# Performance work log

Hardware: AMD Instinct MI355X
Metric: run time of the kernel (lower is better)

## Reference

```python
import jax, jax.numpy as jnp
import numpy as np

# Sampled-neighborhood sizes (NeighborSampler-style shrinking hops)
N0, N1, N2, N3 = 200000, 50000, 12500, 3200
E0, E1, E2 = 500000, 125000, 32000
D_IN, D_H, D_OUT = 128, 256, 128


def setup_inputs() -> dict:
    key = jax.random.key(0)
    ks = jax.random.split(key, 16)
    x = jax.random.normal(ks[0], (N0, D_IN), dtype=jnp.float32)
    src0 = jax.random.randint(ks[1], (E0,), 0, N0)
    dst0 = jax.random.randint(ks[2], (E0,), 0, N1)
    src1 = jax.random.randint(ks[3], (E1,), 0, N1)
    dst1 = jax.random.randint(ks[4], (E1,), 0, N2)
    src2 = jax.random.randint(ks[5], (E2,), 0, N2)
    dst2 = jax.random.randint(ks[6], (E2,), 0, N3)
    s = 0.05
    # SAGEConv params: lin_l (applied to aggregated neighbors, has bias), lin_r (root)
    wl0 = jax.random.normal(ks[7], (D_H, D_IN), dtype=jnp.float32) * s
    wr0 = jax.random.normal(ks[8], (D_H, D_IN), dtype=jnp.float32) * s
    b0 = jnp.zeros((D_H,), dtype=jnp.float32)
    wl1 = jax.random.normal(ks[9], (D_H, D_H), dtype=jnp.float32) * s
    wr1 = jax.random.normal(ks[10], (D_H, D_H), dtype=jnp.float32) * s
    b1 = jnp.zeros((D_H,), dtype=jnp.float32)
    wl2 = jax.random.normal(ks[11], (D_OUT, D_H), dtype=jnp.float32) * s
    wr2 = jax.random.normal(ks[12], (D_OUT, D_H), dtype=jnp.float32) * s
    b2 = jnp.zeros((D_OUT,), dtype=jnp.float32)
    return {"x": x, "src0": src0, "dst0": dst0, "src1": src1, "dst1": dst1,
            "src2": src2, "dst2": dst2,
            "wl0": wl0, "wr0": wr0, "b0": b0,
            "wl1": wl1, "wr1": wr1, "b1": b1,
            "wl2": wl2, "wr2": wr2, "b2": b2}


def _sage(x, src, dst, n_tgt, wl, wr, b):
    """Bipartite SAGEConv with mean aggregation (PyG default)."""
    x_tgt = x[:n_tgt]                                   # [n_tgt, d_in]
    msg = x[src]                                        # [E, d_in] gather
    s = jax.ops.segment_sum(msg, dst, num_segments=n_tgt)
    cnt = jax.ops.segment_sum(jnp.ones((src.shape[0], 1), x.dtype), dst,
                              num_segments=n_tgt)
    mean = s / jnp.maximum(cnt, 1.0)                    # mean over in-neighbors
    return mean @ wl.T + b + x_tgt @ wr.T               # [n_tgt, d_out]


def reference(x, src0, dst0, src1, dst1, src2, dst2,
              wl0, wr0, b0, wl1, wr1, b1, wl2, wr2, b2):
    h = jax.nn.relu(_sage(x, src0, dst0, N1, wl0, wr0, b0))
    h = jax.nn.relu(_sage(h, src1, dst1, N2, wl1, wr1, b1))
    return _sage(h, src2, dst2, N3, wl2, wr2, b2)       # [N3, D_OUT]
```

## Files before the change

kernel.cpp:

```cpp
#include <hip/hip_runtime.h>

#define N0s 200000
#define N1s 50000
#define N2s 12500
#define N3s 3200
#define E0s 500000
#define E1s 125000
#define E2s 32000
#define D_INs 128
#define D_Hs 256
#define D_OUTs 128

#define CAP 32
#define LOGCAP 5

#define GSTRIDE 72

#define WN4 65536
#define WCAST_BLOCKS 32
#define FILLE_BLOCKS ((E0s + E1s + E2s + 255) / 256)

typedef __attribute__((ext_vector_type(8))) short short8;
typedef __attribute__((ext_vector_type(8))) unsigned short ushort8;
typedef __attribute__((ext_vector_type(4))) float floatx4;

__device__ __forceinline__ unsigned short f32_to_bf16_rne(float f) {
    unsigned int u = __float_as_uint(f);
    u += 0x7fffu + ((u >> 16) & 1u);
    return (unsigned short)(u >> 16);
}
__device__ __forceinline__ float bf16_to_f32(unsigned short h) {
    return __uint_as_float(((unsigned int)h) << 16);
}

struct PrepArgs {
    const int *src0, *dst0, *src1, *dst1, *src2, *dst2;
    int *cnt0, *cnt1, *cnt2;
    int *eidx0, *eidx1, *eidx2;
    const float* ws_[6]; unsigned short* wd[6];
};

__launch_bounds__(256)
__global__ void fill3w(PrepArgs a)
{
    if (blockIdx.x < FILLE_BLOCKS) {
        int e = blockIdx.x * 256 + threadIdx.x;
        if (e < E0s) {
            int d = a.dst0[e];
            int p = atomicAdd(&a.cnt0[d], 1);
            if (p < CAP) a.eidx0[(d << LOGCAP) + p] = a.src0[e];
        } else if (e < E0s + E1s) {
            int i = e - E0s;
            int d = a.dst1[i];
            int p = atomicAdd(&a.cnt1[d], 1);
            if (p < CAP) a.eidx1[(d << LOGCAP) + p] = a.src1[i];
        } else if (e < E0s + E1s + E2s) {
            int i = e - E0s - E1s;
            int d = a.dst2[i];
            int p = atomicAdd(&a.cnt2[d], 1);
            if (p < CAP) a.eidx2[(d << LOGCAP) + p] = a.src2[i];
        }
        return;
    }
    int cb = blockIdx.x - FILLE_BLOCKS;
    #pragma unroll
    for (int j = 0; j < 8; ++j) {
        int g = cb * 2048 + j * 256 + threadIdx.x;
        if (g < WN4) {
            int seg, base;
            if      (g < 8192)  { seg = 0; base = 0; }
            else if (g < 16384) { seg = 1; base = 8192; }
            else if (g < 32768) { seg = 2; base = 16384; }
            else if (g < 49152) { seg = 3; base = 32768; }
            else if (g < 57344) { seg = 4; base = 49152; }
            else                { seg = 5; base = 57344; }
            int k = g - base;
            float4 v = *(const float4*)&a.ws_[seg][(size_t)k * 4];
            ushort4 o;
            o.x = f32_to_bf16_rne(v.x);
            o.y = f32_to_bf16_rne(v.y);
            o.z = f32_to_bf16_rne(v.z);
            o.w = f32_to_bf16_rne(v.w);
            *(ushort4*)&a.wd[seg][(size_t)k * 4] = o;
        }
    }
}

__launch_bounds__(256)
__global__ void gather_mean_f32(const float* __restrict__ X,
                                const int* __restrict__ eidx,
                                const int* __restrict__ cnt,
                                unsigned short* __restrict__ out,
                                int n_tgt)
{
    int gid = blockIdx.x * 256 + threadIdx.x;
    int row = gid >> 5;
    if (row >= n_tgt) return;
    int c = (gid & 31) << 2;

    int deg = cnt[row];
    int e = min(deg, CAP);
    const int* bp = &eidx[row << LOGCAP];

    float a0 = 0.f, a1 = 0.f, a2 = 0.f, a3 = 0.f;
    int i = 0;
    for (; i + 4 <= e; i += 4) {
        int4 ss = *(const int4*)&bp[i];
        float4 v0 = *(const float4*)&X[(size_t)ss.x * D_INs + c];
        float4 v1 = *(const float4*)&X[(size_t)ss.y * D_INs + c];
        float4 v2 = *(const float4*)&X[(size_t)ss.z * D_INs + c];
        float4 v3 = *(const float4*)&X[(size_t)ss.w * D_INs + c];
        a0 += (v0.x + v1.x) + (v2.x + v3.x);
        a1 += (v0.y + v1.y) + (v2.y + v3.y);
        a2 += (v0.z + v1.z) + (v2.z + v3.z);
        a3 += (v0.w + v1.w) + (v2.w + v3.w);
    }
    for (; i < e; ++i) {
        float4 v = *(const float4*)&X[(size_t)bp[i] * D_INs + c];
        a0 += v.x; a1 += v.y; a2 += v.z; a3 += v.w;
    }
    float inv = 1.0f / fmaxf((float)deg, 1.0f);
    ushort4 o;
    o.x = f32_to_bf16_rne(a0 * inv);
    o.y = f32_to_bf16_rne(a1 * inv);
    o.z = f32_to_bf16_rne(a2 * inv);
    o.w = f32_to_bf16_rne(a3 * inv);
    *(ushort4*)&out[(size_t)row * D_INs + c] = o;
}

__launch_bounds__(256)
__global__ void gather_mean(const unsigned short* __restrict__ X,
                            const int* __restrict__ eidx,
                            const int* __restrict__ cnt,
                            unsigned short* __restrict__ out,
                            int n_tgt, int D, int shift)
{
    int gid = blockIdx.x * 256 + threadIdx.x;
    int row = gid >> shift;
    if (row >= n_tgt) return;
    int c = (gid & ((1 << shift) - 1)) << 3;

    int deg = cnt[row];
    int e = min(deg, CAP);
    const int* bp = &eidx[row << LOGCAP];

    float acc[8];
    #pragma unroll
    for (int j = 0; j < 8; ++j) acc[j] = 0.f;

    int i = 0;
    for (; i + 4 <= e; i += 4) {
        int4 ss = *(const int4*)&bp[i];
        ushort8 v0 = *(const ushort8*)&X[(size_t)ss.x * D + c];
        ushort8 v1 = *(const ushort8*)&X[(size_t)ss.y * D + c];
        ushort8 v2 = *(const ushort8*)&X[(size_t)ss.z * D + c];
        ushort8 v3 = *(const ushort8*)&X[(size_t)ss.w * D + c];
        #pragma unroll
        for (int j = 0; j < 8; ++j)
            acc[j] += (bf16_to_f32(v0[j]) + bf16_to_f32(v1[j]))
                    + (bf16_to_f32(v2[j]) + bf16_to_f32(v3[j]));
    }
    for (; i < e; ++i) {
        ushort8 v0 = *(const ushort8*)&X[(size_t)bp[i] * D + c];
        #pragma unroll
        for (int j = 0; j < 8; ++j) acc[j] += bf16_to_f32(v0[j]);
    }

    float inv = 1.0f / fmaxf((float)deg, 1.0f);
    ushort8 o;
    #pragma unroll
    for (int j = 0; j < 8; ++j) o[j] = f32_to_bf16_rne(acc[j] * inv);
    *(ushort8*)&out[(size_t)row * D + c] = o;
}

template<int BM, int BN, int OUT_BF16, int RELU, int A2F32>
__launch_bounds__(256)
__global__ void mfma_gemm_t(const unsigned short* __restrict__ A1,
                            const unsigned short* __restrict__ A2,
                            const float* __restrict__ A2f,
                            const unsigned short* __restrict__ W1,
                            const unsigned short* __restrict__ W2,
                            const float* __restrict__ bias,
                            void* __restrict__ Cout,
                            int M, int N, int K1, int K2)
{
    constexpr int MT = BM / 32;
    constexpr int NT = BN / 32;
    constexpr int AITER_A = BM / 32;
    constexpr int AITER_B = BN / 32;
    constexpr int CS = BN + 4;
    constexpr int STAGE_SH = (BM + BN) * GSTRIDE;
    constexpr int CS_SH = OUT_BF16 ? BM * CS : 0;
    constexpr int SMEM_SH = STAGE_SH > CS_SH ? STAGE_SH : CS_SH;

    __shared__ unsigned short smem[SMEM_SH];
    unsigned short* As = smem;
    unsigned short* Bs = smem + BM * GSTRIDE;

    const int tid  = threadIdx.x;
    const int wave = tid >> 6;
    const int lane = tid & 63;
    const int quad = lane >> 4;
    const int lr   = lane & 15;
    const int wm   = wave >> 1;
    const int wn   = wave & 1;
    const int row0 = blockIdx.x * BM;
    const int col0 = blockIdx.y * BN;

    floatx4 acc[MT][NT] = {};

    for (int seg = 0; seg < 2; ++seg) {
        const unsigned short* Wp = (seg == 0) ? W1 : W2;
        const int K = (seg == 0) ? K1 : K2;

        for (int k0 = 0; k0 < K; k0 += 64) {
            if (seg == 1 && A2F32) {
                #pragma unroll
                for (int it = 0; it < BM / 16; ++it) {
                    int sid = tid + it * 256;
                    int r = sid >> 4;
                    int fc = (sid & 15) << 2;
                    int gr = min(row0 + r, M - 1);
                    float4 v = *(const float4*)&A2f[(size_t)gr * K + k0 + fc];
                    ushort4 o;
                    o.x = f32_to_bf16_rne(v.x);
                    o.y = f32_to_bf16_rne(v.y);
                    o.z = f32_to_bf16_rne(v.z);
                    o.w = f32_to_bf16_rne(v.w);
                    *(ushort4*)&As[r * GSTRIDE + fc] = o;
                }
            } else {
                const unsigned short* Ap = (seg == 0) ? A1 : A2;
                #pragma unroll
                for (int it = 0; it < AITER_A; ++it) {
                    int sid = tid + it * 256;
                    int r = sid >> 3;
                    int sc = (sid & 7) << 3;
                    int gr = min(row0 + r, M - 1);
                    uint4 v = *(const uint4*)&Ap[(size_t)gr * K + k0 + sc];
                    *(uint4*)&As[r * GSTRIDE + sc] = v;
                }
            }
            #pragma unroll
            for (int it = 0; it < AITER_B; ++it) {
                int sid = tid + it * 256;
                int r = sid >> 3;
                int sc = (sid & 7) << 3;
                uint4 v = *(const uint4*)&Wp[(size_t)(col0 + r) * K + k0 + sc];
                *(uint4*)&Bs[r * GSTRIDE + sc] = v;
            }
            __syncthreads();

            #pragma unroll
            for (int kh = 0; kh < 2; ++kh) {
                short8 afr[MT], bfr[NT];
                #pragma unroll
                for (int mt = 0; mt < MT; ++mt)
                    afr[mt] = *(const short8*)&As[(wm * (BM/2) + mt * 16 + lr) * GSTRIDE + kh * 32 + quad * 8];
                #pragma unroll
                for (int nt = 0; nt < NT; ++nt)
                    bfr[nt] = *(const short8*)&Bs[(wn * (BN/2) + nt * 16 + lr) * GSTRIDE + kh * 32 + quad * 8];

                #pragma unroll
                for (int mt = 0; mt < MT; ++mt)
                    #pragma unroll
                    for (int nt = 0; nt < NT; ++nt)
                        acc[mt][nt] = __builtin_amdgcn_mfma_f32_16x16x32_bf16(
                            afr[mt], bfr[nt], acc[mt][nt], 0, 0, 0);
            }
            __syncthreads();
        }
    }

    if (OUT_BF16) {
        unsigned short* Cs = smem;
        #pragma unroll
        for (int nt = 0; nt < NT; ++nt) {
            int col = wn * (BN/2) + nt * 16 + lr;
            float bv = bias[col0 + col];
            #pragma unroll
            for (int mt = 0; mt < MT; ++mt) {
                #pragma unroll
                for (int reg = 0; reg < 4; ++reg) {
                    int row = wm * (BM/2) + mt * 16 + quad * 4 + reg;
                    float v = acc[mt][nt][reg] + bv;
                    if (RELU) v = fmaxf(v, 0.f);
                    Cs[row * CS + col] = f32_to_bf16_rne(v);
                }
            }
        }
        __syncthreads();
        constexpr int TPRO = 256 / BM;
        constexpr int SPT  = BN / TPRO;
        int r  = tid / TPRO;
        int hf = tid % TPRO;
        int gr = row0 + r;
        if (gr < M) {
            unsigned short* Crow = (unsigned short*)Cout + (size_t)gr * N + col0 + hf * SPT;
            #pragma unroll
            for (int j = 0; j < SPT / 8; ++j) {
                uint4 v = *(const uint4*)&Cs[r * CS + hf * SPT + j * 8];
                *(uint4*)&Crow[j * 8] = v;
            }
        }
    } else {
        #pragma unroll
        for (int nt = 0; nt < NT; ++nt) {
            int gc = col0 + wn * (BN/2) + nt * 16 + lr;
            float bv = bias[gc];
            #pragma unroll
            for (int mt = 0; mt < MT; ++mt) {
                #pragma unroll
                for (int reg = 0; reg < 4; ++reg) {
                    int gr = row0 + wm * (BM/2) + mt * 16 + quad * 4 + reg;
                    if (gr < M) {
                        float v = acc[mt][nt][reg] + bv;
                        if (RELU) v = fmaxf(v, 0.f);
                        ((float*)Cout)[(size_t)gr * N + gc] = v;
                    }
                }
            }
        }
    }
}

extern "C" void kernel_launch(void* const* d_in, const int* in_sizes, int n_in,
                              void* d_out, int out_size, void* d_ws, size_t ws_size,
                              hipStream_t stream)
{
    const float* x   = (const float*)d_in[0];
    const int* src0  = (const int*)d_in[1];
    const int* dst0  = (const int*)d_in[2];
    const int* src1  = (const int*)d_in[3];
    const int* dst1  = (const int*)d_in[4];
    const int* src2  = (const int*)d_in[5];
    const int* dst2  = (const int*)d_in[6];
    const float* wl0 = (const float*)d_in[7];
    const float* wr0 = (const float*)d_in[8];
    const float* b0  = (const float*)d_in[9];
    const float* wl1 = (const float*)d_in[10];
    const float* wr1 = (const float*)d_in[11];
    const float* b1  = (const float*)d_in[12];
    const float* wl2 = (const float*)d_in[13];
    const float* wr2 = (const float*)d_in[14];
    const float* b2  = (const float*)d_in[15];

    unsigned short* ws = (unsigned short*)d_ws;
    unsigned short* xb    = ws;
    unsigned short* h1    = xb + (size_t)N0s * D_INs;
    unsigned short* h2    = h1 + (size_t)N1s * D_Hs;
    unsigned short* meanA = h2 + (size_t)N2s * D_Hs;
    unsigned short* wl0b  = meanA + (size_t)N1s * D_INs;
    unsigned short* wr0b  = wl0b + 32768;
    unsigned short* wl1b  = wr0b + 32768;
    unsigned short* wr1b  = wl1b + 65536;
    unsigned short* wl2b  = wr1b + 65536;
    unsigned short* wr2b  = wl2b + 32768;
    int* ib = (int*)(wr2b + 32768);
    int* cnt0 = ib;
    int* cnt1 = cnt0 + 50048;
    int* cnt2 = cnt1 + 12544;
    int* eidx0 = cnt2 + 3264;
    int* eidx1 = eidx0 + (size_t)N1s * CAP;
    int* eidx2 = eidx1 + (size_t)N2s * CAP;

    PrepArgs pa;
    pa.src0 = src0; pa.dst0 = dst0; pa.src1 = src1; pa.dst1 = dst1;
    pa.src2 = src2; pa.dst2 = dst2;
    pa.cnt0 = cnt0; pa.cnt1 = cnt1; pa.cnt2 = cnt2;
    pa.eidx0 = eidx0; pa.eidx1 = eidx1; pa.eidx2 = eidx2;
    pa.ws_[0] = wl0; pa.ws_[1] = wr0; pa.ws_[2] = wl1;
    pa.ws_[3] = wr1; pa.ws_[4] = wl2; pa.ws_[5] = wr2;
    pa.wd[0] = wl0b; pa.wd[1] = wr0b; pa.wd[2] = wl1b;
    pa.wd[3] = wr1b; pa.wd[4] = wl2b; pa.wd[5] = wr2b;

    hipMemsetAsync(cnt0, 0, (50048 + 12544 + 3264) * sizeof(int), stream);
    fill3w<<<FILLE_BLOCKS + WCAST_BLOCKS, 256, 0, stream>>>(pa);

    {
        int th = N1s * 32;
        gather_mean_f32<<<(th + 255) / 256, 256, 0, stream>>>(x, eidx0, cnt0,
                                                              meanA, N1s);
        dim3 g((N1s + 127) / 128, D_Hs / 128);
        mfma_gemm_t<128,128,1,1,1><<<g, 256, 0, stream>>>(meanA, nullptr, x,
                                                          wl0b, wr0b, b0, h1,
                                                          N1s, D_Hs, D_INs, D_INs);
    }
    {
        int th = N2s * 32;
        gather_mean<<<(th + 255) / 256, 256, 0, stream>>>(h1, eidx1, cnt1,
                                                          meanA, N2s, D_Hs, 5);
        dim3 g((N2s + 31) / 32, D_Hs / 64);
        mfma_gemm_t<32,64,1,1,0><<<g, 256, 0, stream>>>(meanA, h1, nullptr,
                                                        wl1b, wr1b, b1, h2,
                                                        N2s, D_Hs, D_Hs, D_Hs);
    }
    {
        int th = N3s * 32;
        gather_mean<<<(th + 255) / 256, 256, 0, stream>>>(h2, eidx2, cnt2,
                                                          meanA, N3s, D_Hs, 5);
        dim3 g((N3s + 31) / 32, D_OUTs / 64);
        mfma_gemm_t<32,64,0,0,0><<<g, 256, 0, stream>>>(meanA, h2, nullptr,
                                                        wl2b, wr2b, b2, (float*)d_out,
                                                        N3s, D_OUTs, D_Hs, D_Hs);
    }
}
```

Before: 318.8 us.

## Pre-cast root features to bf16 in prep kernel and retile GEMMs

```diff
diff --git a/kernel.cpp b/kernel.cpp
--- a/kernel.cpp
+++ b/kernel.cpp
@@ -16,8 +16,10 @@
 
 #define GSTRIDE 72
 
+#define XS4 (N1s * D_INs / 4)
 #define WN4 65536
-#define WCAST_BLOCKS 32
+#define CSMALL_TOTAL (XS4 + WN4)
+#define CSMALL_BLOCKS ((CSMALL_TOTAL + 2047) / 2048)
 #define FILLE_BLOCKS ((E0s + E1s + E2s + 255) / 256)
 
 typedef __attribute__((ext_vector_type(8))) short short8;
@@ -37,6 +39,7 @@
     const int *src0, *dst0, *src1, *dst1, *src2, *dst2;
     int *cnt0, *cnt1, *cnt2;
     int *eidx0, *eidx1, *eidx2;
+    const float* x; unsigned short* xb;
     const float* ws_[6]; unsigned short* wd[6];
 };
 
@@ -65,8 +68,17 @@
     int cb = blockIdx.x - FILLE_BLOCKS;
     #pragma unroll
     for (int j = 0; j < 8; ++j) {
-        int g = cb * 2048 + j * 256 + threadIdx.x;
-        if (g < WN4) {
+        int i = cb * 2048 + j * 256 + threadIdx.x;
+        if (i < XS4) {
+            float4 v = *(const float4*)&a.x[(size_t)i * 4];
+            ushort4 o;
+            o.x = f32_to_bf16_rne(v.x);
+            o.y = f32_to_bf16_rne(v.y);
+            o.z = f32_to_bf16_rne(v.z);
+            o.w = f32_to_bf16_rne(v.w);
+            *(ushort4*)&a.xb[(size_t)i * 4] = o;
+        } else if (i < CSMALL_TOTAL) {
+            int g = i - XS4;
             int seg, base;
             if      (g < 8192)  { seg = 0; base = 0; }
             else if (g < 16384) { seg = 1; base = 8192; }
@@ -173,11 +185,10 @@
     *(ushort8*)&out[(size_t)row * D + c] = o;
 }
 
-template<int BM, int BN, int OUT_BF16, int RELU, int A2F32>
+template<int BM, int BN, int OUT_BF16, int RELU>
 __launch_bounds__(256)
 __global__ void mfma_gemm_t(const unsigned short* __restrict__ A1,
                             const unsigned short* __restrict__ A2,
-                            const float* __restrict__ A2f,
                             const unsigned short* __restrict__ W1,
                             const unsigned short* __restrict__ W2,
                             const float* __restrict__ bias,
@@ -210,36 +221,19 @@
     floatx4 acc[MT][NT] = {};
 
     for (int seg = 0; seg < 2; ++seg) {
+        const unsigned short* Ap = (seg == 0) ? A1 : A2;
         const unsigned short* Wp = (seg == 0) ? W1 : W2;
         const int K = (seg == 0) ? K1 : K2;
 
         for (int k0 = 0; k0 < K; k0 += 64) {
-            if (seg == 1 && A2F32) {
-                #pragma unroll
-                for (int it = 0; it < BM / 16; ++it) {
-                    int sid = tid + it * 256;
-                    int r = sid >> 4;
-                    int fc = (sid & 15) << 2;
-                    int gr = min(row0 + r, M - 1);
-                    float4 v = *(const float4*)&A2f[(size_t)gr * K + k0 + fc];
-                    ushort4 o;
-                    o.x = f32_to_bf16_rne(v.x);
-                    o.y = f32_to_bf16_rne(v.y);
-                    o.z = f32_to_bf16_rne(v.z);
-                    o.w = f32_to_bf16_rne(v.w);
-                    *(ushort4*)&As[r * GSTRIDE + fc] = o;
-                }
-            } else {
-                const unsigned short* Ap = (seg == 0) ? A1 : A2;
-                #pragma unroll
-                for (int it = 0; it < AITER_A; ++it) {
-                    int sid = tid + it * 256;
-                    int r = sid >> 3;
-                    int sc = (sid & 7) << 3;
-                    int gr = min(row0 + r, M - 1);
-                    uint4 v = *(const uint4*)&Ap[(size_t)gr * K + k0 + sc];
-                    *(uint4*)&As[r * GSTRIDE + sc] = v;
-                }
+            #pragma unroll
+            for (int it = 0; it < AITER_A; ++it) {
+                int sid = tid + it * 256;
+                int r = sid >> 3;
+                int sc = (sid & 7) << 3;
+                int gr = min(row0 + r, M - 1);
+                uint4 v = *(const uint4*)&Ap[(size_t)gr * K + k0 + sc];
+                *(uint4*)&As[r * GSTRIDE + sc] = v;
             }
             #pragma unroll
             for (int it = 0; it < AITER_B; ++it) {
@@ -369,39 +363,37 @@
     pa.src2 = src2; pa.dst2 = dst2;
     pa.cnt0 = cnt0; pa.cnt1 = cnt1; pa.cnt2 = cnt2;
     pa.eidx0 = eidx0; pa.eidx1 = eidx1; pa.eidx2 = eidx2;
+    pa.x = x; pa.xb = xb;
     pa.ws_[0] = wl0; pa.ws_[1] = wr0; pa.ws_[2] = wl1;
     pa.ws_[3] = wr1; pa.ws_[4] = wl2; pa.ws_[5] = wr2;
     pa.wd[0] = wl0b; pa.wd[1] = wr0b; pa.wd[2] = wl1b;
     pa.wd[3] = wr1b; pa.wd[4] = wl2b; pa.wd[5] = wr2b;
 
     hipMemsetAsync(cnt0, 0, (50048 + 12544 + 3264) * sizeof(int), stream);
-    fill3w<<<FILLE_BLOCKS + WCAST_BLOCKS, 256, 0, stream>>>(pa);
+    fill3w<<<FILLE_BLOCKS + CSMALL_BLOCKS, 256, 0, stream>>>(pa);
 
     {
         int th = N1s * 32;
         gather_mean_f32<<<(th + 255) / 256, 256, 0, stream>>>(x, eidx0, cnt0,
                                                               meanA, N1s);
-        dim3 g((N1s + 127) / 128, D_Hs / 128);
-        mfma_gemm_t<128,128,1,1,1><<<g, 256, 0, stream>>>(meanA, nullptr, x,
-                                                          wl0b, wr0b, b0, h1,
-                                                          N1s, D_Hs, D_INs, D_INs);
+        dim3 g((N1s + 63) / 64, 1);
+        mfma_gemm_t<64,256,1,1><<<g, 256, 0, stream>>>(meanA, xb, wl0b, wr0b, b0, h1,
+                                                       N1s, D_Hs, D_INs, D_INs);
     }
     {
         int th = N2s * 32;
         gather_mean<<<(th + 255) / 256, 256, 0, stream>>>(h1, eidx1, cnt1,
                                                           meanA, N2s, D_Hs, 5);
-        dim3 g((N2s + 31) / 32, D_Hs / 64);
-        mfma_gemm_t<32,64,1,1,0><<<g, 256, 0, stream>>>(meanA, h1, nullptr,
-                                                        wl1b, wr1b, b1, h2,
-                                                        N2s, D_Hs, D_Hs, D_Hs);
+        dim3 g((N2s + 63) / 64, D_Hs / 64);
+        mfma_gemm_t<64,64,1,1><<<g, 256, 0, stream>>>(meanA, h1, wl1b, wr1b, b1, h2,
+                                                      N2s, D_Hs, D_Hs, D_Hs);
     }
     {
         int th = N3s * 32;
         gather_mean<<<(th + 255) / 256, 256, 0, stream>>>(h2, eidx2, cnt2,
                                                           meanA, N3s, D_Hs, 5);
-        dim3 g((N3s + 31) / 32, D_OUTs / 64);
-        mfma_gemm_t<32,64,0,0,0><<<g, 256, 0, stream>>>(meanA, h2, nullptr,
-                                                        wl2b, wr2b, b2, (float*)d_out,
-                                                        N3s, D_OUTs, D_Hs, D_Hs);
-    }
-}
+        dim3 g((N3s + 63) / 64, D_OUTs / 64);
+        mfma_gemm_t<64,64,0,0><<<g, 256, 0, stream>>>(meanA, h2, wl2b, wr2b, b2, (float*)d_out,
+                                                      N3s, D_OUTs, D_Hs, D_Hs);
+    }
+}
```

Measured after the change: 322.8 us. About the same (+1.3%).
